# Kernel tuning notes

Hardware: AMD Instinct MI355X
Metric: run time of the kernel (lower is better)

## Reference

```python
import jax, jax.numpy as jnp
import numpy as np

N_UNITS = 512
INPUT_DIM = 128
OUT_CLASSES = 10
BATCH = 128
T = 1024
EPS = 0.01
BETA = 0.8
GAMMA = 0.01
ALPHA = 1.0


def setup_inputs() -> dict:
    key = jax.random.key(0)
    ks = jax.random.split(key, 7)
    x = jax.random.normal(ks[0], (BATCH, T, INPUT_DIM), dtype=jnp.float32)
    # gaussian_init_(n, std=1) ~ N(0, 1/n) per entry (std/sqrt(n))
    s = 1.0 / np.sqrt(N_UNITS)
    B = jax.random.normal(ks[1], (N_UNITS, N_UNITS), dtype=jnp.float32) * s
    C = jax.random.normal(ks[2], (N_UNITS, N_UNITS), dtype=jnp.float32) * s
    E_w = jax.random.normal(ks[3], (INPUT_DIM, N_UNITS), dtype=jnp.float32) / np.sqrt(INPUT_DIM)
    E_b = jnp.zeros((N_UNITS,), dtype=jnp.float32)
    D_w = jax.random.normal(ks[4], (N_UNITS, OUT_CLASSES), dtype=jnp.float32) / np.sqrt(N_UNITS)
    D_b = jnp.zeros((OUT_CLASSES,), dtype=jnp.float32)
    return {"x": x, "B": B, "C": C, "E_w": E_w, "E_b": E_b, "D_w": D_w, "D_b": D_b}


def reference(x, B, C, E_w, E_b, D_w, D_b):
    n = B.shape[0]
    I = jnp.eye(n, dtype=x.dtype)
    # A, W built once (i == 0 branch in torch loop)
    A = BETA * (B - B.T) + (1.0 - BETA) * (B + B.T) - GAMMA * I
    W = BETA * (C - C.T) + (1.0 - BETA) * (C + C.T) - GAMMA * I
    # precompute input projections for all timesteps: [B, T, n]
    z_all = jnp.einsum('bti,in->btn', x, E_w) + E_b
    h0 = jnp.zeros((x.shape[0], n), dtype=x.dtype)

    def step(h, z):
        h_new = h + EPS * ALPHA * (h @ A) + EPS * jnp.tanh(h @ W + z)
        return h_new, None

    h_final, _ = jax.lax.scan(step, h0, jnp.swapaxes(z_all, 0, 1))  # scan over T
    out = h_final @ D_w + D_b
    return out
```

## Files before the change

### kernel.cpp

```cpp
#include <hip/hip_runtime.h>
#include <math.h>

#define NU 512
#define BT 128
#define TT 1024
#define ID 128
#define OC 10
#define GGRP 32
#define CWG 8
#define RROW 4
#define JCOL 64
#define THREADS 512

static constexpr float F_EPS = 0.01f;
static constexpr float F_CT  = -0.6f;
static constexpr float F_GAM = 0.01f;

#define WS_HX1 131072

#define OFF_H  0
#define OFF_X0 2176
#define OFF_X1 2816
#define LDS_BYTES 98304

typedef float f32x4 __attribute__((ext_vector_type(4)));
typedef float f32x2 __attribute__((ext_vector_type(2)));
typedef int   i32x4 __attribute__((ext_vector_type(4)));
typedef int   i32x2 __attribute__((ext_vector_type(2)));

__global__ void init_kernel(float* ws) {
    int i = blockIdx.x * 256 + threadIdx.x;
    *(f32x4*)(ws + (size_t)i * 4) = (f32x4){0.f, 0.f, 0.f, 0.f};
}

__global__ __launch_bounds__(THREADS, 2)
void scan_kernel(const float* __restrict__ x, const float* __restrict__ B,
                 const float* __restrict__ C, const float* __restrict__ Ew,
                 const float* __restrict__ Eb, float* ws)
{
    extern __shared__ float sm[];
    const int tid = threadIdx.x;
    const int bid = blockIdx.x;
    const int g = bid & (GGRP - 1);
    const int slice = bid >> 5;
    const int jbase = slice * JCOL;
    const int row0 = g * RROW;

    unsigned* hx0 = (unsigned*)ws;
    unsigned* hx1 = (unsigned*)ws + WS_HX1;

    const int lane = tid & 63;
    const int w = tid >> 6;
    const int jl = lane & 7;
    const int kc = lane >> 3;
    const int cg = jbase + w * 8 + jl;
    const int k0 = kc * 64;

    f32x2 rA[32], rW[32], rE[8];
    #pragma unroll
    for (int u2 = 0; u2 < 32; ++u2) {
        #pragma unroll
        for (int p = 0; p < 2; ++p) {
            int k = k0 + 2 * u2 + p;
            float dia = (k == cg) ? F_GAM : 0.0f;
            rA[u2][p] = B[(size_t)k * NU + cg] + F_CT * B[(size_t)cg * NU + k] - dia;
            rW[u2][p] = C[(size_t)k * NU + cg] + F_CT * C[(size_t)cg * NU + k] - dia;
        }
    }
    #pragma unroll
    for (int v2 = 0; v2 < 8; ++v2) {
        rE[v2][0] = Ew[(size_t)(kc * 16 + 2 * v2) * NU + cg];
        rE[v2][1] = Ew[(size_t)(kc * 16 + 2 * v2 + 1) * NU + cg];
    }
    const float ebv = Eb[cg];

    const int sr = tid >> 7;
    const int sk = (tid & 127) * 4;
    const int xi = tid & 127;
    const int hp = sr * 544 + sk + (sk >> 6) * 4;
    const int xp = sr * 160 + xi + (xi >> 4) * 4;
    const size_t xrow = (size_t)(row0 + sr) * TT * ID;
    const size_t pbase = ((size_t)(row0 + sr) * NU + sk) * 2;

    sm[OFF_X0 + xp] = x[xrow + xi];
    __syncthreads();

    for (int t = 0; t < TT; ++t) {
        const unsigned* hxin = (t & 1) ? hx1 : hx0;
        unsigned* hxout = (t & 1) ? hx0 : hx1;
        const int xcur = (t & 1) ? OFF_X1 : OFF_X0;
        const int xnxt = (t & 1) ? OFF_X0 : OFF_X1;

        f32x4 hvv;
        {
            const unsigned* src = hxin + pbase;
            i32x4 p0, p1;
            for (;;) {
                asm volatile("global_load_dwordx4 %0, %2, off sc0 sc1\n\t"
                             "global_load_dwordx4 %1, %3, off sc0 sc1\n\t"
                             "s_waitcnt vmcnt(0)"
                             : "=&v"(p0), "=&v"(p1)
                             : "v"(src), "v"(src + 4) : "memory");
                if (p0[1] == t && p0[3] == t && p1[1] == t && p1[3] == t)
                    break;
                __builtin_amdgcn_s_sleep(1);
            }
            hvv[0] = __int_as_float(p0[0]);
            hvv[1] = __int_as_float(p0[2]);
            hvv[2] = __int_as_float(p1[0]);
            hvv[3] = __int_as_float(p1[2]);
        }

        *(f32x4*)(sm + OFF_H + hp) = hvv;
        float xnv;
        {
            const int tn = (t + 1 < TT) ? (t + 1) : t;
            const float* xsrc = x + xrow + (size_t)tn * ID + xi;
            asm volatile("global_load_dword %0, %1, off"
                         : "=v"(xnv) : "v"(xsrc));
        }
        __syncthreads();

        f32x2 zac[RROW];
        #pragma unroll
        for (int r = 0; r < RROW; ++r) {
            zac[r] = (f32x2){0.f, 0.f};
            const float* xr = sm + xcur + r * 160 + kc * 20;
            #pragma unroll
            for (int q = 0; q < 4; ++q) {
                f32x4 xv = *(const f32x4*)(xr + q * 4);
                f32x2 xlo = __builtin_shufflevector(xv, xv, 0, 1);
                f32x2 xhi = __builtin_shufflevector(xv, xv, 2, 3);
                zac[r] = __builtin_elementwise_fma(xlo, rE[2 * q], zac[r]);
                zac[r] = __builtin_elementwise_fma(xhi, rE[2 * q + 1], zac[r]);
            }
        }

        f32x2 aA[RROW], aW[RROW];
        #pragma unroll
        for (int r = 0; r < RROW; ++r) {
            aA[r] = (f32x2){0.f, 0.f};
            aW[r] = zac[r];
            const float* hr = sm + OFF_H + r * 544 + kc * 68;
            #pragma unroll
            for (int q = 0; q < 16; ++q) {
                f32x4 hv = *(const f32x4*)(hr + q * 4);
                f32x2 hlo = __builtin_shufflevector(hv, hv, 0, 1);
                f32x2 hhi = __builtin_shufflevector(hv, hv, 2, 3);
                aA[r] = __builtin_elementwise_fma(hlo, rA[2 * q], aA[r]);
                aW[r] = __builtin_elementwise_fma(hlo, rW[2 * q], aW[r]);
                aA[r] = __builtin_elementwise_fma(hhi, rA[2 * q + 1], aA[r]);
                aW[r] = __builtin_elementwise_fma(hhi, rW[2 * q + 1], aW[r]);
            }
        }

        float sA[RROW], sW[RROW];
        #pragma unroll
        for (int r = 0; r < RROW; ++r) {
            sA[r] = aA[r][0] + aA[r][1];
            sW[r] = aW[r][0] + aW[r][1];
        }
        #pragma unroll
        for (int m = 8; m <= 32; m <<= 1) {
            #pragma unroll
            for (int r = 0; r < RROW; ++r) {
                sA[r] += __shfl_xor(sA[r], m, 64);
                sW[r] += __shfl_xor(sW[r], m, 64);
            }
        }

        if (kc < RROW) {
            int r = kc;
            float hold = sm[OFF_H + r * 544 + cg + (cg >> 6) * 4];
            float hnew = hold + F_EPS * sA[r] + F_EPS * tanhf(sW[r] + ebv);
            i32x2 pv;
            pv[0] = __float_as_int(hnew);
            pv[1] = t + 1;
            unsigned* dst = hxout + ((size_t)(row0 + r) * NU + cg) * 2;
            asm volatile("global_store_dwordx2 %0, %1, off sc0 sc1"
                         :: "v"(dst), "v"(pv) : "memory");
        }

        asm volatile("s_waitcnt vmcnt(1)" : "+v"(xnv) :: "memory");
        if (t + 1 < TT)
            sm[xnxt + xp] = xnv;

        __syncthreads();
    }
}

__global__ void head_kernel(const float* __restrict__ ws, const float* __restrict__ Dw,
                            const float* __restrict__ Db, float* __restrict__ out)
{
    __shared__ float red2[32][16];
    int b = blockIdx.x;
    int tid = threadIdx.x;
    int j = tid & 15;
    int kc = tid >> 4;
    const float* h = ws;
    float acc = 0.0f;
    if (j < OC) {
        for (int u = 0; u < 16; ++u) {
            int k = kc * 16 + u;
            acc += h[((size_t)b * NU + k) * 2] * Dw[(size_t)k * OC + j];
        }
    }
    red2[kc][j] = acc;
    __syncthreads();
    if (kc == 0 && j < OC) {
        float s = 0.0f;
        #pragma unroll
        for (int u = 0; u < 32; ++u) s += red2[u][j];
        out[(size_t)b * OC + j] = s + Db[j];
    }
}

extern "C" void kernel_launch(void* const* d_in, const int* in_sizes, int n_in,
                              void* d_out, int out_size, void* d_ws, size_t ws_size,
                              hipStream_t stream) {
    const float* x  = (const float*)d_in[0];
    const float* B  = (const float*)d_in[1];
    const float* C  = (const float*)d_in[2];
    const float* Ew = (const float*)d_in[3];
    const float* Eb = (const float*)d_in[4];
    const float* Dw = (const float*)d_in[5];
    const float* Db = (const float*)d_in[6];
    float* ws  = (float*)d_ws;
    float* out = (float*)d_out;

    (void)hipFuncSetAttribute((const void*)scan_kernel,
                              hipFuncAttributeMaxDynamicSharedMemorySize, LDS_BYTES);

    init_kernel<<<256, 256, 0, stream>>>(ws);
    scan_kernel<<<GGRP * CWG, THREADS, LDS_BYTES, stream>>>(x, B, C, Ew, Eb, ws);
    head_kernel<<<BT, THREADS, 0, stream>>>(ws, Dw, Db, out);
}
```

Measured before the change: 3.702 ms.

## Assign two columns per lane and reduce partial sums with DPP

```diff
diff --git a/kernel.cpp b/kernel.cpp
--- a/kernel.cpp
+++ b/kernel.cpp
@@ -26,7 +26,10 @@
 typedef float f32x4 __attribute__((ext_vector_type(4)));
 typedef float f32x2 __attribute__((ext_vector_type(2)));
 typedef int   i32x4 __attribute__((ext_vector_type(4)));
-typedef int   i32x2 __attribute__((ext_vector_type(2)));
+
+#define DPP_ADD(v, CTRL) \
+    ((v) + __int_as_float(__builtin_amdgcn_update_dpp( \
+        0, __float_as_int(v), CTRL, 0xF, 0xF, true)))
 
 __global__ void init_kernel(float* ws) {
     int i = blockIdx.x * 256 + threadIdx.x;
@@ -51,28 +54,35 @@
 
     const int lane = tid & 63;
     const int w = tid >> 6;
-    const int jl = lane & 7;
-    const int kc = lane >> 3;
-    const int cg = jbase + w * 8 + jl;
-    const int k0 = kc * 64;
-
-    f32x2 rA[32], rW[32], rE[8];
+    const int kc = (lane & 3) | ((lane & 0x18) >> 1);
+    const int jl = ((lane >> 2) & 1) | ((lane >> 4) & 2);
+    const int cg0 = jbase + w * 8 + jl * 2;
+    const int k0 = kc * 32;
+    const int i0 = kc * 8;
+
+    f32x2 rA[2][16], rW[2][16], rE[2][4];
     #pragma unroll
-    for (int u2 = 0; u2 < 32; ++u2) {
-        #pragma unroll
-        for (int p = 0; p < 2; ++p) {
-            int k = k0 + 2 * u2 + p;
-            float dia = (k == cg) ? F_GAM : 0.0f;
-            rA[u2][p] = B[(size_t)k * NU + cg] + F_CT * B[(size_t)cg * NU + k] - dia;
-            rW[u2][p] = C[(size_t)k * NU + cg] + F_CT * C[(size_t)cg * NU + k] - dia;
-        }
-    }
-    #pragma unroll
-    for (int v2 = 0; v2 < 8; ++v2) {
-        rE[v2][0] = Ew[(size_t)(kc * 16 + 2 * v2) * NU + cg];
-        rE[v2][1] = Ew[(size_t)(kc * 16 + 2 * v2 + 1) * NU + cg];
-    }
-    const float ebv = Eb[cg];
+    for (int c = 0; c < 2; ++c) {
+        const int cgc = cg0 + c;
+        #pragma unroll
+        for (int u2 = 0; u2 < 16; ++u2) {
+            #pragma unroll
+            for (int p = 0; p < 2; ++p) {
+                int k = k0 + 2 * u2 + p;
+                float dia = (k == cgc) ? F_GAM : 0.0f;
+                rA[c][u2][p] = B[(size_t)k * NU + cgc] + F_CT * B[(size_t)cgc * NU + k] - dia;
+                rW[c][u2][p] = C[(size_t)k * NU + cgc] + F_CT * C[(size_t)cgc * NU + k] - dia;
+            }
+        }
+        #pragma unroll
+        for (int p2 = 0; p2 < 4; ++p2) {
+            rE[c][p2][0] = Ew[(size_t)(i0 + 2 * p2) * NU + cgc];
+            rE[c][p2][1] = Ew[(size_t)(i0 + 2 * p2 + 1) * NU + cgc];
+        }
+    }
+    f32x2 ebv;
+    ebv[0] = Eb[cg0];
+    ebv[1] = Eb[cg0 + 1];
 
     const int sr = tid >> 7;
     const int sk = (tid & 127) * 4;
@@ -121,63 +131,91 @@
         }
         __syncthreads();
 
-        f32x2 zac[RROW];
+        f32x2 aA[RROW][2], aW[RROW][2];
         #pragma unroll
         for (int r = 0; r < RROW; ++r) {
-            zac[r] = (f32x2){0.f, 0.f};
-            const float* xr = sm + xcur + r * 160 + kc * 20;
-            #pragma unroll
-            for (int q = 0; q < 4; ++q) {
-                f32x4 xv = *(const f32x4*)(xr + q * 4);
-                f32x2 xlo = __builtin_shufflevector(xv, xv, 0, 1);
-                f32x2 xhi = __builtin_shufflevector(xv, xv, 2, 3);
-                zac[r] = __builtin_elementwise_fma(xlo, rE[2 * q], zac[r]);
-                zac[r] = __builtin_elementwise_fma(xhi, rE[2 * q + 1], zac[r]);
-            }
-        }
-
-        f32x2 aA[RROW], aW[RROW];
-        #pragma unroll
-        for (int r = 0; r < RROW; ++r) {
-            aA[r] = (f32x2){0.f, 0.f};
-            aW[r] = zac[r];
-            const float* hr = sm + OFF_H + r * 544 + kc * 68;
-            #pragma unroll
-            for (int q = 0; q < 16; ++q) {
+            const float* xr = sm + xcur + r * 160 + i0 + (kc >> 1) * 4;
+            f32x4 xv0 = *(const f32x4*)(xr);
+            f32x4 xv1 = *(const f32x4*)(xr + 4);
+            f32x2 xl0 = __builtin_shufflevector(xv0, xv0, 0, 1);
+            f32x2 xh0 = __builtin_shufflevector(xv0, xv0, 2, 3);
+            f32x2 xl1 = __builtin_shufflevector(xv1, xv1, 0, 1);
+            f32x2 xh1 = __builtin_shufflevector(xv1, xv1, 2, 3);
+            #pragma unroll
+            for (int c = 0; c < 2; ++c) {
+                f32x2 z = (f32x2){0.f, 0.f};
+                z = __builtin_elementwise_fma(xl0, rE[c][0], z);
+                z = __builtin_elementwise_fma(xh0, rE[c][1], z);
+                z = __builtin_elementwise_fma(xl1, rE[c][2], z);
+                z = __builtin_elementwise_fma(xh1, rE[c][3], z);
+                aW[r][c] = z;
+                aA[r][c] = (f32x2){0.f, 0.f};
+            }
+            const float* hr = sm + OFF_H + r * 544 + k0 + (kc >> 1) * 4;
+            #pragma unroll
+            for (int q = 0; q < 8; ++q) {
                 f32x4 hv = *(const f32x4*)(hr + q * 4);
                 f32x2 hlo = __builtin_shufflevector(hv, hv, 0, 1);
                 f32x2 hhi = __builtin_shufflevector(hv, hv, 2, 3);
-                aA[r] = __builtin_elementwise_fma(hlo, rA[2 * q], aA[r]);
-                aW[r] = __builtin_elementwise_fma(hlo, rW[2 * q], aW[r]);
-                aA[r] = __builtin_elementwise_fma(hhi, rA[2 * q + 1], aA[r]);
-                aW[r] = __builtin_elementwise_fma(hhi, rW[2 * q + 1], aW[r]);
-            }
-        }
-
-        float sA[RROW], sW[RROW];
-        #pragma unroll
-        for (int r = 0; r < RROW; ++r) {
-            sA[r] = aA[r][0] + aA[r][1];
-            sW[r] = aW[r][0] + aW[r][1];
-        }
-        #pragma unroll
-        for (int m = 8; m <= 32; m <<= 1) {
-            #pragma unroll
-            for (int r = 0; r < RROW; ++r) {
-                sA[r] += __shfl_xor(sA[r], m, 64);
-                sW[r] += __shfl_xor(sW[r], m, 64);
-            }
-        }
-
-        if (kc < RROW) {
-            int r = kc;
-            float hold = sm[OFF_H + r * 544 + cg + (cg >> 6) * 4];
-            float hnew = hold + F_EPS * sA[r] + F_EPS * tanhf(sW[r] + ebv);
-            i32x2 pv;
-            pv[0] = __float_as_int(hnew);
+                #pragma unroll
+                for (int c = 0; c < 2; ++c) {
+                    aA[r][c] = __builtin_elementwise_fma(hlo, rA[c][2 * q], aA[r][c]);
+                    aW[r][c] = __builtin_elementwise_fma(hlo, rW[c][2 * q], aW[r][c]);
+                    aA[r][c] = __builtin_elementwise_fma(hhi, rA[c][2 * q + 1], aA[r][c]);
+                    aW[r][c] = __builtin_elementwise_fma(hhi, rW[c][2 * q + 1], aW[r][c]);
+                }
+            }
+        }
+
+        float sA[RROW][2], sW[RROW][2];
+        #pragma unroll
+        for (int r = 0; r < RROW; ++r)
+            #pragma unroll
+            for (int c = 0; c < 2; ++c) {
+                sA[r][c] = aA[r][c][0] + aA[r][c][1];
+                sW[r][c] = aW[r][c][0] + aW[r][c][1];
+            }
+        #pragma unroll
+        for (int r = 0; r < RROW; ++r)
+            #pragma unroll
+            for (int c = 0; c < 2; ++c) {
+                sA[r][c] = DPP_ADD(sA[r][c], 0xB1);
+                sW[r][c] = DPP_ADD(sW[r][c], 0xB1);
+            }
+        #pragma unroll
+        for (int r = 0; r < RROW; ++r)
+            #pragma unroll
+            for (int c = 0; c < 2; ++c) {
+                sA[r][c] = DPP_ADD(sA[r][c], 0x4E);
+                sW[r][c] = DPP_ADD(sW[r][c], 0x4E);
+            }
+        #pragma unroll
+        for (int r = 0; r < RROW; ++r)
+            #pragma unroll
+            for (int c = 0; c < 2; ++c) {
+                sA[r][c] = DPP_ADD(sA[r][c], 0x128);
+                sW[r][c] = DPP_ADD(sW[r][c], 0x128);
+            }
+        #pragma unroll
+        for (int r = 0; r < RROW; ++r)
+            #pragma unroll
+            for (int c = 0; c < 2; ++c) {
+                sA[r][c] += __shfl_xor(sA[r][c], 16, 64);
+                sW[r][c] += __shfl_xor(sW[r][c], 16, 64);
+            }
+
+        if ((lane & 0x18) == 0) {
+            const int r = lane & 3;
+            const f32x2 hold = *(const f32x2*)(sm + OFF_H + r * 544 + cg0 + (cg0 >> 6) * 4);
+            float h0n = hold[0] + F_EPS * sA[r][0] + F_EPS * tanhf(sW[r][0] + ebv[0]);
+            float h1n = hold[1] + F_EPS * sA[r][1] + F_EPS * tanhf(sW[r][1] + ebv[1]);
+            i32x4 pv;
+            pv[0] = __float_as_int(h0n);
             pv[1] = t + 1;
-            unsigned* dst = hxout + ((size_t)(row0 + r) * NU + cg) * 2;
-            asm volatile("global_store_dwordx2 %0, %1, off sc0 sc1"
+            pv[2] = __float_as_int(h1n);
+            pv[3] = t + 1;
+            unsigned* dst = hxout + ((size_t)(row0 + r) * NU + cg0) * 2;
+            asm volatile("global_store_dwordx4 %0, %1, off sc0 sc1"
                          :: "v"(dst), "v"(pv) : "memory");
         }
 
```

New measurement: 4.257 ms. 15.0% more time.

## Pipeline per-row h polling with compute across four phases per timestep

Applied to the files above, without the earlier changes.

```diff
diff --git a/kernel.cpp b/kernel.cpp
--- a/kernel.cpp
+++ b/kernel.cpp
@@ -25,7 +25,6 @@
 
 typedef float f32x4 __attribute__((ext_vector_type(4)));
 typedef float f32x2 __attribute__((ext_vector_type(2)));
-typedef int   i32x4 __attribute__((ext_vector_type(4)));
 typedef int   i32x2 __attribute__((ext_vector_type(2)));
 
 __global__ void init_kernel(float* ws) {
@@ -33,7 +32,60 @@
     *(f32x4*)(ws + (size_t)i * 4) = (f32x4){0.f, 0.f, 0.f, 0.f};
 }
 
-__global__ __launch_bounds__(THREADS, 2)
+#define PH_CHECK(PP, NW, SRCP)                                               \
+    asm volatile("s_waitcnt vmcnt(" #NW ")" : "+v"(PP) :: "memory");         \
+    while ((PP)[1] != t) {                                                   \
+        __builtin_amdgcn_s_sleep(1);                                         \
+        asm volatile("global_load_dwordx2 %0, %1, off sc0 sc1\n\t"           \
+                     "s_waitcnt vmcnt(0)"                                    \
+                     : "=&v"(PP) : "v"(SRCP) : "memory");                    \
+    }
+
+#define PH_ISSUE(PP, SRCP)                                                   \
+    asm volatile("global_load_dwordx2 %0, %1, off sc0 sc1"                   \
+                 : "=&v"(PP) : "v"(SRCP) : "memory");
+
+#define PH_COMPUTE(R)                                                        \
+    {                                                                        \
+        f32x2 z = (f32x2){0.f, 0.f};                                         \
+        const float* xr = sm + xcur + (R) * 160 + kc * 20;                   \
+        _Pragma("unroll")                                                    \
+        for (int q = 0; q < 4; ++q) {                                        \
+            f32x4 xv = *(const f32x4*)(xr + q * 4);                          \
+            f32x2 xlo = __builtin_shufflevector(xv, xv, 0, 1);               \
+            f32x2 xhi = __builtin_shufflevector(xv, xv, 2, 3);               \
+            z = __builtin_elementwise_fma(xlo, rE[2 * q], z);                \
+            z = __builtin_elementwise_fma(xhi, rE[2 * q + 1], z);            \
+        }                                                                    \
+        f32x2 aA = (f32x2){0.f, 0.f};                                        \
+        f32x2 aW = z;                                                        \
+        const float* hr = sm + OFF_H + (R) * 544 + kc * 68;                  \
+        _Pragma("unroll")                                                    \
+        for (int q = 0; q < 16; ++q) {                                       \
+            f32x4 hv = *(const f32x4*)(hr + q * 4);                          \
+            f32x2 hlo = __builtin_shufflevector(hv, hv, 0, 1);               \
+            f32x2 hhi = __builtin_shufflevector(hv, hv, 2, 3);               \
+            aA = __builtin_elementwise_fma(hlo, rA[2 * q], aA);              \
+            aW = __builtin_elementwise_fma(hlo, rW[2 * q], aW);              \
+            aA = __builtin_elementwise_fma(hhi, rA[2 * q + 1], aA);          \
+            aW = __builtin_elementwise_fma(hhi, rW[2 * q + 1], aW);          \
+        }                                                                    \
+        float sA = aA[0] + aA[1], sW = aW[0] + aW[1];                        \
+        sA += __shfl_xor(sA, 8, 64);  sW += __shfl_xor(sW, 8, 64);           \
+        sA += __shfl_xor(sA, 16, 64); sW += __shfl_xor(sW, 16, 64);          \
+        sA += __shfl_xor(sA, 32, 64); sW += __shfl_xor(sW, 32, 64);          \
+        if (lane < 8) {                                                      \
+            float hold = sm[OFF_H + (R) * 544 + cg + (cg >> 6) * 4];         \
+            float hnew = hold + F_EPS * sA + F_EPS * tanhf(sW + ebv);        \
+            i32x2 pv; pv[0] = __float_as_int(hnew); pv[1] = t + 1;           \
+            unsigned* dst = hxout + ((size_t)(row0 + (R)) * NU + cg) * 2;    \
+            asm volatile("global_store_dwordx2 %0, %1, off sc0 sc1"          \
+                         :: "v"(dst), "v"(pv) : "memory");                   \
+        }                                                                    \
+    }
+
+__global__ __launch_bounds__(THREADS)
+__attribute__((amdgpu_waves_per_eu(2, 2)))
 void scan_kernel(const float* __restrict__ x, const float* __restrict__ B,
                  const float* __restrict__ C, const float* __restrict__ Ew,
                  const float* __restrict__ Eb, float* ws)
@@ -74,118 +126,75 @@
     }
     const float ebv = Eb[cg];
 
+    const int hcol = tid + (tid >> 6) * 4;
+    const size_t pb0 = ((size_t)(row0 + 0) * NU + tid) * 2;
+    const size_t pb1 = ((size_t)(row0 + 1) * NU + tid) * 2;
+    const size_t pb2 = ((size_t)(row0 + 2) * NU + tid) * 2;
+    const size_t pb3 = ((size_t)(row0 + 3) * NU + tid) * 2;
+
     const int sr = tid >> 7;
-    const int sk = (tid & 127) * 4;
     const int xi = tid & 127;
-    const int hp = sr * 544 + sk + (sk >> 6) * 4;
     const int xp = sr * 160 + xi + (xi >> 4) * 4;
     const size_t xrow = (size_t)(row0 + sr) * TT * ID;
-    const size_t pbase = ((size_t)(row0 + sr) * NU + sk) * 2;
 
     sm[OFF_X0 + xp] = x[xrow + xi];
     __syncthreads();
+    i32x2 ppA, ppB;
+    {
+        const unsigned* p0 = hx0 + pb0;
+        asm volatile("global_load_dwordx2 %0, %1, off sc0 sc1\n\t"
+                     "s_waitcnt vmcnt(0)"
+                     : "=&v"(ppA) : "v"(p0) : "memory");
+    }
 
     for (int t = 0; t < TT; ++t) {
         const unsigned* hxin = (t & 1) ? hx1 : hx0;
         unsigned* hxout = (t & 1) ? hx0 : hx1;
         const int xcur = (t & 1) ? OFF_X1 : OFF_X0;
         const int xnxt = (t & 1) ? OFF_X0 : OFF_X1;
-
-        f32x4 hvv;
-        {
-            const unsigned* src = hxin + pbase;
-            i32x4 p0, p1;
-            for (;;) {
-                asm volatile("global_load_dwordx4 %0, %2, off sc0 sc1\n\t"
-                             "global_load_dwordx4 %1, %3, off sc0 sc1\n\t"
-                             "s_waitcnt vmcnt(0)"
-                             : "=&v"(p0), "=&v"(p1)
-                             : "v"(src), "v"(src + 4) : "memory");
-                if (p0[1] == t && p0[3] == t && p1[1] == t && p1[3] == t)
-                    break;
-                __builtin_amdgcn_s_sleep(1);
-            }
-            hvv[0] = __int_as_float(p0[0]);
-            hvv[1] = __int_as_float(p0[2]);
-            hvv[2] = __int_as_float(p1[0]);
-            hvv[3] = __int_as_float(p1[2]);
-        }
-
-        *(f32x4*)(sm + OFF_H + hp) = hvv;
         float xnv;
-        {
+
+        {
+            const unsigned* p0 = hxin + pb0;
+            PH_CHECK(ppA, 1, p0)
+            const unsigned* p1 = hxin + pb1;
+            PH_ISSUE(ppB, p1)
             const int tn = (t + 1 < TT) ? (t + 1) : t;
             const float* xsrc = x + xrow + (size_t)tn * ID + xi;
-            asm volatile("global_load_dword %0, %1, off"
-                         : "=v"(xnv) : "v"(xsrc));
-        }
-        __syncthreads();
-
-        f32x2 zac[RROW];
-        #pragma unroll
-        for (int r = 0; r < RROW; ++r) {
-            zac[r] = (f32x2){0.f, 0.f};
-            const float* xr = sm + xcur + r * 160 + kc * 20;
-            #pragma unroll
-            for (int q = 0; q < 4; ++q) {
-                f32x4 xv = *(const f32x4*)(xr + q * 4);
-                f32x2 xlo = __builtin_shufflevector(xv, xv, 0, 1);
-                f32x2 xhi = __builtin_shufflevector(xv, xv, 2, 3);
-                zac[r] = __builtin_elementwise_fma(xlo, rE[2 * q], zac[r]);
-                zac[r] = __builtin_elementwise_fma(xhi, rE[2 * q + 1], zac[r]);
-            }
-        }
-
-        f32x2 aA[RROW], aW[RROW];
-        #pragma unroll
-        for (int r = 0; r < RROW; ++r) {
-            aA[r] = (f32x2){0.f, 0.f};
-            aW[r] = zac[r];
-            const float* hr = sm + OFF_H + r * 544 + kc * 68;
-            #pragma unroll
-            for (int q = 0; q < 16; ++q) {
-                f32x4 hv = *(const f32x4*)(hr + q * 4);
-                f32x2 hlo = __builtin_shufflevector(hv, hv, 0, 1);
-                f32x2 hhi = __builtin_shufflevector(hv, hv, 2, 3);
-                aA[r] = __builtin_elementwise_fma(hlo, rA[2 * q], aA[r]);
-                aW[r] = __builtin_elementwise_fma(hlo, rW[2 * q], aW[r]);
-                aA[r] = __builtin_elementwise_fma(hhi, rA[2 * q + 1], aA[r]);
-                aW[r] = __builtin_elementwise_fma(hhi, rW[2 * q + 1], aW[r]);
-            }
-        }
-
-        float sA[RROW], sW[RROW];
-        #pragma unroll
-        for (int r = 0; r < RROW; ++r) {
-            sA[r] = aA[r][0] + aA[r][1];
-            sW[r] = aW[r][0] + aW[r][1];
-        }
-        #pragma unroll
-        for (int m = 8; m <= 32; m <<= 1) {
-            #pragma unroll
-            for (int r = 0; r < RROW; ++r) {
-                sA[r] += __shfl_xor(sA[r], m, 64);
-                sW[r] += __shfl_xor(sW[r], m, 64);
-            }
-        }
-
-        if (kc < RROW) {
-            int r = kc;
-            float hold = sm[OFF_H + r * 544 + cg + (cg >> 6) * 4];
-            float hnew = hold + F_EPS * sA[r] + F_EPS * tanhf(sW[r] + ebv);
-            i32x2 pv;
-            pv[0] = __float_as_int(hnew);
-            pv[1] = t + 1;
-            unsigned* dst = hxout + ((size_t)(row0 + r) * NU + cg) * 2;
-            asm volatile("global_store_dwordx2 %0, %1, off sc0 sc1"
-                         :: "v"(dst), "v"(pv) : "memory");
-        }
-
-        asm volatile("s_waitcnt vmcnt(1)" : "+v"(xnv) :: "memory");
-        if (t + 1 < TT)
-            sm[xnxt + xp] = xnv;
-
-        __syncthreads();
+            asm volatile("global_load_dword %0, %1, off" : "=v"(xnv) : "v"(xsrc));
+            sm[OFF_H + 0 * 544 + hcol] = __int_as_float(ppA[0]);
+            __syncthreads();
+            PH_COMPUTE(0)
+        }
+        {
+            const unsigned* p1 = hxin + pb1;
+            PH_CHECK(ppB, 2, p1)
+            const unsigned* p2 = hxin + pb2;
+            PH_ISSUE(ppA, p2)
+            sm[OFF_H + 1 * 544 + hcol] = __int_as_float(ppB[0]);
+            __syncthreads();
+            PH_COMPUTE(1)
+        }
+        {
+            const unsigned* p2 = hxin + pb2;
+            PH_CHECK(ppA, 1, p2)
+            const unsigned* p3 = hxin + pb3;
+            PH_ISSUE(ppB, p3)
+            sm[OFF_H + 2 * 544 + hcol] = __int_as_float(ppA[0]);
+            __syncthreads();
+            PH_COMPUTE(2)
+        }
+        {
+            const unsigned* p3 = hxin + pb3;
+            PH_CHECK(ppB, 1, p3)
+            const unsigned* p0n = hxout + pb0;
+            PH_ISSUE(ppA, p0n)
+            if (t + 1 < TT)
+                sm[xnxt + xp] = xnv;
+            sm[OFF_H + 3 * 544 + hcol] = __int_as_float(ppB[0]);
+            __syncthreads();
+            PH_COMPUTE(3)
+        }
     }
 }
 
```

Result: faster. 3.547 ms (-4.2%).
